# Kernel optimization log

Hardware: AMD Instinct MI355X
Metric: run time of the kernel (lower is better)

## Reference

```python
import jax, jax.numpy as jnp
import numpy as np

N = 100000
E = 3200000
IN_C, H1, H2 = 512, 64, 32


def gcn_norm(edge_index, edge_weight, num_nodes):
    """PyG gcn_norm with add_self_loops=True: D^-1/2 (A+I) D^-1/2 edge weights."""
    row, col = edge_index[0], edge_index[1]
    loop = jnp.arange(num_nodes, dtype=edge_index.dtype)
    row = jnp.concatenate([row, loop])
    col = jnp.concatenate([col, loop])
    w = jnp.concatenate([edge_weight, jnp.ones((num_nodes,), edge_weight.dtype)])
    deg = jax.ops.segment_sum(w, col, num_segments=num_nodes)
    dinv = jnp.where(deg > 0, jax.lax.rsqrt(jnp.maximum(deg, 1e-12)), 0.0)
    wnorm = dinv[row] * w * dinv[col]
    return row, col, wnorm


def gcn_conv(x, W, b, row, col, wnorm, num_nodes):
    h = x @ W                                   # [N, out] linear first (out <= in)
    msg = wnorm[:, None] * h[row]               # gather + per-edge scale  [E+N, out]
    out = jax.ops.segment_sum(msg, col, num_segments=num_nodes)
    return out + b


def setup_inputs() -> dict:
    key = jax.random.key(0)
    ks = jax.random.split(key, 9)
    x = jax.random.normal(ks[0], (N, IN_C), dtype=jnp.float32)
    edge_index = jax.random.randint(ks[1], (2, E), 0, N, dtype=jnp.int64)
    edge_weight = jax.random.uniform(ks[2], (E,), dtype=jnp.float32)
    # Glorot-style init for GCN linear weights, zero bias (PyG defaults).
    def glorot(k, fan_in, fan_out):
        s = np.sqrt(6.0 / (fan_in + fan_out)).astype(np.float32)
        return jax.random.uniform(k, (fan_in, fan_out), jnp.float32, -s, s)
    return {
        "x": x,
        "edge_index": edge_index,
        "edge_weight": edge_weight,
        "W1": glorot(ks[3], IN_C, H1), "b1": jnp.zeros((H1,), jnp.float32),
        "W2": glorot(ks[4], H1, H2),  "b2": jnp.zeros((H2,), jnp.float32),
        "W3": glorot(ks[5], H2, 1),   "b3": jnp.zeros((1,), jnp.float32),
    }


def reference(x, edge_index, edge_weight, W1, b1, W2, b2, W3, b3):
    # Inference mode: dropout is identity (training=False).
    row, col, wnorm = gcn_norm(edge_index, edge_weight, N)  # cached=True: shared across layers
    h = jax.nn.relu(gcn_conv(x, W1, b1, row, col, wnorm, N))
    h = jax.nn.relu(gcn_conv(h, W2, b2, row, col, wnorm, N))
    h = gcn_conv(h, W3, b3, row, col, wnorm, N)
    return h.reshape(-1)  # [N]
```

## Files before the change

kernel.cpp:

```cpp
#include <hip/hip_runtime.h>

constexpr int BLK = 256;
constexpr int NBLKBIN = 512;
constexpr int MAXNB   = 1024;

typedef __bf16 bf16x8 __attribute__((ext_vector_type(8)));
typedef float  f32x4  __attribute__((ext_vector_type(4)));

__device__ __forceinline__ float blo(unsigned u) { return __uint_as_float(u << 16); }
__device__ __forceinline__ float bhi(unsigned u) { return __uint_as_float(u & 0xffff0000u); }

__device__ __forceinline__ int detect64(const void* ei) {
    const int* p = (const int*)ei;
    int is64 = 1;
#pragma unroll
    for (int i = 0; i < 16; ++i)
        if (p[2 * i + 1] != 0) is64 = 0;
    return is64;
}

__device__ __forceinline__ int load_idx(const void* ei, size_t pos, int is64) {
    if (is64) return (int)((const long long*)ei)[pos];
    return ((const int*)ei)[pos];
}

__global__ void k_prep(const float* __restrict__ W1, const float* __restrict__ W2,
                       __bf16* __restrict__ Wtf, __bf16* __restrict__ Wtf2,
                       int* __restrict__ bkt_cnt, int nb) {
    const int b = blockIdx.x;
    const int t = threadIdx.x;
    if (b < 16) {
        int i = b * 256 + t;
        int lane = i & 63;
        int tt   = (i >> 6) & 3;
        int k0c  = i >> 8;
        int col  = tt * 16 + (lane & 15);
        int kbase = k0c * 32 + (lane >> 4) * 8;
        bf16x8 v;
#pragma unroll
        for (int j = 0; j < 8; ++j) v[j] = (__bf16)W1[(size_t)(kbase + j) * 64 + col];
        *(bf16x8*)(Wtf + (size_t)i * 8) = v;
    } else if (b == 16) {
        int i = t;
        int lane = i & 63;
        int ct   = i >> 6;
        int tt = ct & 1, chunk = ct >> 1;
        int col  = tt * 16 + (lane & 15);
        int kbase = chunk * 32 + (lane >> 4) * 8;
        bf16x8 v;
#pragma unroll
        for (int j = 0; j < 8; ++j) v[j] = (__bf16)W2[(size_t)(kbase + j) * 32 + col];
        *(bf16x8*)(Wtf2 + (size_t)i * 8) = v;
    } else {
        for (int i = t; i < nb; i += 256) bkt_cnt[i] = 0;
    }
}

__global__ __launch_bounds__(256) void k_binhist(const void* __restrict__ ei, int e,
                                                 int* __restrict__ bucket_cnt, int nb) {
    __shared__ int hist[MAXNB];
    const int t = threadIdx.x;
    for (int b = t; b < nb; b += 256) hist[b] = 0;
    __syncthreads();
    const int is64 = detect64(ei);
    const int chunk = (e + NBLKBIN - 1) / NBLKBIN;
    const int i0 = blockIdx.x * chunk;
    const int i1 = min(e, i0 + chunk);
    for (int i = i0 + t; i < i1; i += 256) {
        int dst = load_idx(ei, (size_t)e + i, is64);
        atomicAdd(&hist[dst >> 7], 1);
    }
    __syncthreads();
    for (int b = t; b < nb; b += 256) {
        int c = hist[b];
        if (c) atomicAdd(&bucket_cnt[b], c);
    }
}

__global__ void k_scanbkt(const int* __restrict__ cnt, int* __restrict__ offs,
                          int* __restrict__ cursor, int nb, int e) {
    __shared__ int sh[256];
    const int t = threadIdx.x;
    const int base = t * 4;
    int v[4]; int s = 0;
#pragma unroll
    for (int k = 0; k < 4; ++k) {
        int i = base + k;
        v[k] = (i < nb) ? cnt[i] : 0;
        s += v[k];
    }
    sh[t] = s;
    __syncthreads();
    for (int d = 1; d < 256; d <<= 1) {
        int x = (t >= d) ? sh[t - d] : 0;
        __syncthreads();
        sh[t] += x;
        __syncthreads();
    }
    int excl = (t == 0) ? 0 : sh[t - 1];
#pragma unroll
    for (int k = 0; k < 4; ++k) {
        int i = base + k;
        if (i < nb) { offs[i] = excl; cursor[i] = excl; excl += v[k]; }
    }
    if (t == 255) offs[nb] = e;
}

__global__ __launch_bounds__(256) void k_binscatter(const void* __restrict__ ei,
                                                    const float* __restrict__ ew, int e,
                                                    int* __restrict__ bucket_cursor,
                                                    int2* __restrict__ binned, int nb) {
    __shared__ int hist[MAXNB];
    const int t = threadIdx.x;
    for (int b = t; b < nb; b += 256) hist[b] = 0;
    __syncthreads();
    const int is64 = detect64(ei);
    const int chunk = (e + NBLKBIN - 1) / NBLKBIN;
    const int i0 = blockIdx.x * chunk;
    const int i1 = min(e, i0 + chunk);
    for (int i = i0 + t; i < i1; i += 256) {
        int dst = load_idx(ei, (size_t)e + i, is64);
        atomicAdd(&hist[dst >> 7], 1);
    }
    __syncthreads();
    for (int b = t; b < nb; b += 256) {
        int c = hist[b];
        int base = 0;
        if (c) base = atomicAdd(&bucket_cursor[b], c);
        hist[b] = base;
    }
    __syncthreads();
    for (int i = i0 + t; i < i1; i += 256) {
        int dst = load_idx(ei, (size_t)e + i, is64);
        int src = load_idx(ei, (size_t)i, is64);
        float w = ew[i];
        int bin = dst >> 7;
        int pos = atomicAdd(&hist[bin], 1);
        binned[pos] = make_int2(src | ((dst & 127) << 20), __float_as_int(w));
    }
}

__global__ __launch_bounds__(256) void k_bucketcnt(const int* __restrict__ bucket_offs,
                                                   const int2* __restrict__ binned,
                                                   int* __restrict__ counts,
                                                   float* __restrict__ dinv, int n) {
    __shared__ int                icnt[128];
    __shared__ unsigned long long facc[128];
    const int t = threadIdx.x;
    const int k = blockIdx.x;
    if (t < 128) { icnt[t] = 0; facc[t] = 0ull; }
    __syncthreads();
    const int j0 = bucket_offs[k], j1 = bucket_offs[k + 1];
    const float SCALE = 1099511627776.f;
    for (int j = j0 + t; j < j1; j += 256) {
        int2 p = binned[j];
        int dl = ((unsigned)p.x) >> 20;
        atomicAdd(&icnt[dl], 1);
        atomicAdd(&facc[dl], (unsigned long long)(__int_as_float(p.y) * SCALE));
    }
    __syncthreads();
    if (t < 128) {
        int nd = k * 128 + t;
        if (nd < n) {
            counts[nd] = icnt[t];
            float deg = fmaf((float)facc[t], 1.f / 1099511627776.f, 1.0f);
            dinv[nd] = rsqrtf(deg);
        }
    }
}

__global__ void k_scan1(const int* __restrict__ in, int* __restrict__ out,
                        int* __restrict__ bsum, int n) {
    __shared__ int sh[256];
    const int t = threadIdx.x;
    const int base = blockIdx.x * 1024 + t * 4;
    int v[4];
    int s = 0;
#pragma unroll
    for (int k = 0; k < 4; ++k) {
        int i = base + k;
        v[k] = (i < n) ? in[i] : 0;
        s += v[k];
    }
    sh[t] = s;
    __syncthreads();
    for (int d = 1; d < 256; d <<= 1) {
        int x = (t >= d) ? sh[t - d] : 0;
        __syncthreads();
        sh[t] += x;
        __syncthreads();
    }
    int excl = (t == 0) ? 0 : sh[t - 1];
    if (t == 255) bsum[blockIdx.x] = sh[255];
#pragma unroll
    for (int k = 0; k < 4; ++k) {
        int i = base + k;
        if (i < n) { out[i] = excl; excl += v[k]; }
    }
}

__global__ void k_scan2(int* __restrict__ bsum, int nb) {
    __shared__ int sh[128];
    const int t = threadIdx.x;
    sh[t] = (t < nb) ? bsum[t] : 0;
    __syncthreads();
    for (int d = 1; d < 128; d <<= 1) {
        int x = (t >= d) ? sh[t - d] : 0;
        __syncthreads();
        sh[t] += x;
        __syncthreads();
    }
    if (t < nb) bsum[t] = (t == 0) ? 0 : sh[t - 1];
}

__global__ void k_scan3(int* __restrict__ offs, const int* __restrict__ scanned,
                        const int* __restrict__ bsum, int n, int e) {
    long i = (long)blockIdx.x * BLK + threadIdx.x;
    if (i < n) offs[i] = scanned[i] + bsum[i >> 10];
    if (i == 0) offs[n] = e;
}

__global__ __launch_bounds__(256) void k_place(const int* __restrict__ bucket_offs,
                                               const int2* __restrict__ binned,
                                               const int* __restrict__ offs,
                                               const float* __restrict__ dinv,
                                               int2* __restrict__ csrp, int n) {
    __shared__ int cur[128];
    const int t = threadIdx.x;
    const int k = blockIdx.x;
    if (t < 128) {
        int nd = k * 128 + t;
        cur[t] = (nd < n) ? offs[nd] : 0;
    }
    __syncthreads();
    const int j0 = bucket_offs[k], j1 = bucket_offs[k + 1];
    for (int j = j0 + t; j < j1; j += 256) {
        int2 p = binned[j];
        int dl  = ((unsigned)p.x) >> 20;
        int src = p.x & 0xFFFFF;
        int pos = atomicAdd(&cur[dl], 1);
        float w2 = __int_as_float(p.y) * dinv[src];
        csrp[pos] = make_int2(src, __float_as_int(w2));
    }
}

__global__ __launch_bounds__(256) void k_gemm1_mfma(const float* __restrict__ X,
                                                    const __bf16* __restrict__ Wtf,
                                                    __bf16* __restrict__ H, int nrows) {
    const int wave = threadIdx.x >> 6;
    const int lane = threadIdx.x & 63;
    const int l15  = lane & 15;
    const int lq   = lane >> 4;
    const long rbase = (long)blockIdx.x * 128 + wave * 32;

    long ar0 = rbase + l15;      if (ar0 >= nrows) ar0 = nrows - 1;
    long ar1 = rbase + 16 + l15; if (ar1 >= nrows) ar1 = nrows - 1;
    const float4* x0 = (const float4*)(X + (size_t)ar0 * 512) + lq * 2;
    const float4* x1 = (const float4*)(X + (size_t)ar1 * 512) + lq * 2;

    f32x4 acc[2][4];
#pragma unroll
    for (int r = 0; r < 2; ++r)
#pragma unroll
        for (int t = 0; t < 4; ++t) acc[r][t] = f32x4{0.f, 0.f, 0.f, 0.f};

    float4 pa[2][2][2];
#pragma unroll
    for (int s = 0; s < 2; ++s) {
        pa[s][0][0] = x0[s * 8]; pa[s][0][1] = x0[s * 8 + 1];
        pa[s][1][0] = x1[s * 8]; pa[s][1][1] = x1[s * 8 + 1];
    }

#pragma unroll
    for (int k0c = 0; k0c < 16; ++k0c) {
        const int s = k0c & 1;
        float4 a00 = pa[s][0][0], a01 = pa[s][0][1];
        float4 a10 = pa[s][1][0], a11 = pa[s][1][1];
        if (k0c + 2 < 16) {
            pa[s][0][0] = x0[(k0c + 2) * 8]; pa[s][0][1] = x0[(k0c + 2) * 8 + 1];
            pa[s][1][0] = x1[(k0c + 2) * 8]; pa[s][1][1] = x1[(k0c + 2) * 8 + 1];
        }
        bf16x8 af0, af1;
        af0[0] = (__bf16)a00.x; af0[1] = (__bf16)a00.y; af0[2] = (__bf16)a00.z; af0[3] = (__bf16)a00.w;
        af0[4] = (__bf16)a01.x; af0[5] = (__bf16)a01.y; af0[6] = (__bf16)a01.z; af0[7] = (__bf16)a01.w;
        af1[0] = (__bf16)a10.x; af1[1] = (__bf16)a10.y; af1[2] = (__bf16)a10.z; af1[3] = (__bf16)a10.w;
        af1[4] = (__bf16)a11.x; af1[5] = (__bf16)a11.y; af1[6] = (__bf16)a11.z; af1[7] = (__bf16)a11.w;
#pragma unroll
        for (int t = 0; t < 4; ++t) {
            bf16x8 bf_ = *(const bf16x8*)(Wtf + ((size_t)(k0c * 4 + t) * 64 + lane) * 8);
            acc[0][t] = __builtin_amdgcn_mfma_f32_16x16x32_bf16(af0, bf_, acc[0][t], 0, 0, 0);
            acc[1][t] = __builtin_amdgcn_mfma_f32_16x16x32_bf16(af1, bf_, acc[1][t], 0, 0, 0);
        }
    }
#pragma unroll
    for (int rr = 0; rr < 2; ++rr)
#pragma unroll
    for (int t = 0; t < 4; ++t)
#pragma unroll
    for (int r = 0; r < 4; ++r) {
        long row = rbase + rr * 16 + lq * 4 + r;
        if (row < nrows) H[(size_t)row * 64 + t * 16 + l15] = (__bf16)acc[rr][t][r];
    }
}

__global__ __launch_bounds__(256) void k_gemm2_mfma(const __bf16* __restrict__ A,
                                                    const __bf16* __restrict__ Wtf2,
                                                    __bf16* __restrict__ H, int nrows) {
    const int wave = threadIdx.x >> 6;
    const int lane = threadIdx.x & 63;
    const int l15  = lane & 15;
    const int lq   = lane >> 4;
    const long rbase = (long)blockIdx.x * 64 + wave * 16;

    long arow = rbase + l15;
    if (arow >= nrows) arow = nrows - 1;

    f32x4 acc[2] = {{0.f,0.f,0.f,0.f},{0.f,0.f,0.f,0.f}};
#pragma unroll
    for (int c = 0; c < 2; ++c) {
        bf16x8 af = *(const bf16x8*)(A + (size_t)arow * 64 + c * 32 + lq * 8);
#pragma unroll
        for (int t = 0; t < 2; ++t) {
            bf16x8 bf_ = *(const bf16x8*)(Wtf2 + ((size_t)(c * 2 + t) * 64 + lane) * 8);
            acc[t] = __builtin_amdgcn_mfma_f32_16x16x32_bf16(af, bf_, acc[t], 0, 0, 0);
        }
    }
#pragma unroll
    for (int t = 0; t < 2; ++t)
#pragma unroll
    for (int r = 0; r < 4; ++r) {
        long row = rbase + lq * 4 + r;
        if (row < nrows) H[(size_t)row * 32 + t * 16 + l15] = (__bf16)acc[t][r];
    }
}

template <int K, int EPI>
__global__ __launch_bounds__(256) void k_prop_bf(const int* __restrict__ offs,
                                                 const int2* __restrict__ csrp,
                                                 const __bf16* __restrict__ hb,
                                                 const float* __restrict__ dinv,
                                                 const float* __restrict__ bias,
                                                 const float* __restrict__ W3,
                                                 void* __restrict__ outv, int n) {
    constexpr int SUB = K / 4;
    constexpr int NPW = 64 / SUB;
    constexpr int NPB = 4 * NPW;
    const int t    = threadIdx.x;
    const int lane = t & 63;
    const int wave = t >> 6;
    const int chq  = lane & (SUB - 1);
    const int sub  = lane / SUB;
    const long nd  = (long)blockIdx.x * NPB + wave * NPW + sub;
    if (nd >= n) return;

    const unsigned short* h = (const unsigned short*)hb;
    const int j0 = offs[nd], j1 = offs[nd + 1];
    float a0 = 0.f, a1 = 0.f, a2 = 0.f, a3 = 0.f;
    int j = j0;
    for (; j + 3 < j1; j += 4) {
        int2 p0 = csrp[j];
        int2 p1 = csrp[j + 1];
        int2 p2 = csrp[j + 2];
        int2 p3 = csrp[j + 3];
        uint2 u0 = *(const uint2*)(h + (size_t)p0.x * K + 4 * chq);
        uint2 u1 = *(const uint2*)(h + (size_t)p1.x * K + 4 * chq);
        uint2 u2 = *(const uint2*)(h + (size_t)p2.x * K + 4 * chq);
        uint2 u3 = *(const uint2*)(h + (size_t)p3.x * K + 4 * chq);
        float w0 = __int_as_float(p0.y), w1 = __int_as_float(p1.y);
        float w2 = __int_as_float(p2.y), w3 = __int_as_float(p3.y);
        a0 = fmaf(w0, blo(u0.x), a0); a1 = fmaf(w0, bhi(u0.x), a1);
        a2 = fmaf(w0, blo(u0.y), a2); a3 = fmaf(w0, bhi(u0.y), a3);
        a0 = fmaf(w1, blo(u1.x), a0); a1 = fmaf(w1, bhi(u1.x), a1);
        a2 = fmaf(w1, blo(u1.y), a2); a3 = fmaf(w1, bhi(u1.y), a3);
        a0 = fmaf(w2, blo(u2.x), a0); a1 = fmaf(w2, bhi(u2.x), a1);
        a2 = fmaf(w2, blo(u2.y), a2); a3 = fmaf(w2, bhi(u2.y), a3);
        a0 = fmaf(w3, blo(u3.x), a0); a1 = fmaf(w3, bhi(u3.x), a1);
        a2 = fmaf(w3, blo(u3.y), a2); a3 = fmaf(w3, bhi(u3.y), a3);
    }
    for (; j < j1; ++j) {
        int2 p0 = csrp[j];
        uint2 u0 = *(const uint2*)(h + (size_t)p0.x * K + 4 * chq);
        float w0 = __int_as_float(p0.y);
        a0 = fmaf(w0, blo(u0.x), a0); a1 = fmaf(w0, bhi(u0.x), a1);
        a2 = fmaf(w0, blo(u0.y), a2); a3 = fmaf(w0, bhi(u0.y), a3);
    }
    const float di = dinv[nd];
    const float s  = di * di;
    uint2 us = *(const uint2*)(h + (size_t)nd * K + 4 * chq);
    float4 bv = *(const float4*)(bias + 4 * chq);
    float o0 = fmaf(di, a0, fmaf(s, blo(us.x), bv.x));
    float o1 = fmaf(di, a1, fmaf(s, bhi(us.x), bv.y));
    float o2 = fmaf(di, a2, fmaf(s, blo(us.y), bv.z));
    float o3 = fmaf(di, a3, fmaf(s, bhi(us.y), bv.w));
    o0 = fmaxf(o0, 0.f); o1 = fmaxf(o1, 0.f); o2 = fmaxf(o2, 0.f); o3 = fmaxf(o3, 0.f);
    if (EPI == 0) {
        unsigned short s0 = __builtin_bit_cast(unsigned short, (__bf16)o0);
        unsigned short s1 = __builtin_bit_cast(unsigned short, (__bf16)o1);
        unsigned short s2 = __builtin_bit_cast(unsigned short, (__bf16)o2);
        unsigned short s3 = __builtin_bit_cast(unsigned short, (__bf16)o3);
        uint2 pk;
        pk.x = (unsigned)s0 | ((unsigned)s1 << 16);
        pk.y = (unsigned)s2 | ((unsigned)s3 << 16);
        *(uint2*)((unsigned*)outv + (size_t)nd * (K / 2) + 2 * chq) = pk;
    } else {
        float4 wv = *(const float4*)(W3 + 4 * chq);
        float part = o0 * wv.x + o1 * wv.y + o2 * wv.z + o3 * wv.w;
#pragma unroll
        for (int d = SUB / 2; d >= 1; d >>= 1) part += __shfl_xor(part, d, SUB);
        if (chq == 0) ((float*)outv)[nd] = part;
    }
}

__global__ __launch_bounds__(256) void k_prop1(const int* __restrict__ offs,
                                               const int2* __restrict__ csrp,
                                               const float* __restrict__ h,
                                               const float* __restrict__ dinv,
                                               const float* __restrict__ bias,
                                               float* __restrict__ out, int n) {
    long nd = (long)blockIdx.x * BLK + threadIdx.x;
    if (nd >= n) return;
    const int j0 = offs[nd], j1 = offs[nd + 1];
    float acc = 0.f;
    int j = j0;
    for (; j + 3 < j1; j += 4) {
        int2 p0 = csrp[j];
        int2 p1 = csrp[j + 1];
        int2 p2 = csrp[j + 2];
        int2 p3 = csrp[j + 3];
        acc = fmaf(__int_as_float(p0.y), h[p0.x], acc);
        acc = fmaf(__int_as_float(p1.y), h[p1.x], acc);
        acc = fmaf(__int_as_float(p2.y), h[p2.x], acc);
        acc = fmaf(__int_as_float(p3.y), h[p3.x], acc);
    }
    for (; j < j1; ++j) {
        int2 p0 = csrp[j];
        acc = fmaf(__int_as_float(p0.y), h[p0.x], acc);
    }
    const float di = dinv[nd];
    out[nd] = fmaf(di, acc, fmaf(di * di, h[nd], bias[0]));
}

extern "C" void kernel_launch(void* const* d_in, const int* in_sizes, int n_in,
                              void* d_out, int out_size, void* d_ws, size_t ws_size,
                              hipStream_t stream) {
    const float* x  = (const float*)d_in[0];
    const void*  ei = d_in[1];
    const float* ew = (const float*)d_in[2];
    const float* W1 = (const float*)d_in[3];
    const float* b1 = (const float*)d_in[4];
    const float* W2 = (const float*)d_in[5];
    const float* b2 = (const float*)d_in[6];
    const float* W3 = (const float*)d_in[7];
    const float* b3 = (const float*)d_in[8];
    float* out = (float*)d_out;

    const int n = in_sizes[0] / 512;
    const int e = in_sizes[2];
    const int nb = (n + 127) >> 7;

    char* ws = (char*)d_ws;
    size_t off = 0;
    auto alloc = [&](size_t bytes) {
        void* p = ws + off;
        off = (off + bytes + 255) & ~(size_t)255;
        return p;
    };
    int2*   binned   = (int2*)  alloc((size_t)e * 8);
    __bf16* hbuf1    = (__bf16*)binned;
    int*    bkt_cnt  = (int*)   alloc((size_t)(MAXNB + 1) * 4);
    int*    bkt_offs = (int*)   alloc((size_t)(MAXNB + 1) * 4);
    int*    bkt_cur  = (int*)   alloc((size_t)(MAXNB + 1) * 4);
    int*    counts   = (int*)   alloc((size_t)n * 4);
    int*    offs     = (int*)   alloc((size_t)(n + 1) * 4);
    int*    bsum     = (int*)   alloc(512);
    int2*   csrp     = (int2*)  alloc((size_t)e * 8);
    float*  dinv     = (float*) alloc((size_t)n * 4);
    __bf16* pb64     = (__bf16*)alloc((size_t)n * 64 * 2);
    __bf16* hbuf2    = (__bf16*)alloc((size_t)n * 32 * 2);
    float*  h3       = (float*) alloc((size_t)n * 4);
    __bf16* Wtf      = (__bf16*)alloc((size_t)512 * 64 * 2);
    __bf16* Wtf2     = (__bf16*)alloc((size_t)64 * 32 * 2);
    (void)ws_size; (void)n_in; (void)out_size;

    const int gb_n = (n + BLK - 1) / BLK;
    const int nb_scan = (n + 1023) / 1024;

    k_prep<<<18, 256, 0, stream>>>(W1, W2, Wtf, Wtf2, bkt_cnt, nb);
    k_binhist<<<NBLKBIN, 256, 0, stream>>>(ei, e, bkt_cnt, nb);
    k_scanbkt<<<1, 256, 0, stream>>>(bkt_cnt, bkt_offs, bkt_cur, nb, e);
    k_binscatter<<<NBLKBIN, 256, 0, stream>>>(ei, ew, e, bkt_cur, binned, nb);
    k_bucketcnt<<<nb, 256, 0, stream>>>(bkt_offs, binned, counts, dinv, n);
    k_scan1<<<nb_scan, 256, 0, stream>>>(counts, counts, bsum, n);
    k_scan2<<<1, 128, 0, stream>>>(bsum, nb_scan);
    k_scan3<<<gb_n, BLK, 0, stream>>>(offs, counts, bsum, n, e);
    k_place<<<nb, 256, 0, stream>>>(bkt_offs, binned, offs, dinv, csrp, n);

    k_gemm1_mfma<<<(n + 127) / 128, 256, 0, stream>>>(x, Wtf, hbuf1, n);
    k_prop_bf<64, 0><<<(n + 15) / 16, 256, 0, stream>>>(offs, csrp, hbuf1, dinv, b1, nullptr, pb64, n);

    k_gemm2_mfma<<<(n + 63) / 64, 256, 0, stream>>>(pb64, Wtf2, hbuf2, n);
    k_prop_bf<32, 1><<<(n + 31) / 32, 256, 0, stream>>>(offs, csrp, hbuf2, dinv, b2, W3, h3, n);

    k_prop1<<<gb_n, BLK, 0, stream>>>(offs, csrp, h3, dinv, b3, out, n);
}
```

Measured before the change: 349.0 us.

## Fuse CSR build into one kernel and fold source dinv into GEMM outputs

Merges the bucket count, three-kernel global scan and placement into a single per-bucket kernel. Because buckets are contiguous in the binned array, each bucket's offsets come from its own start plus a local 128-entry scan. The source-side D^-1/2 scaling moves out of the per-edge weights and into the GEMM epilogues (and the layer-3 projection), so CSR placement no longer needs a random gather of dinv per edge. This removes four launches and a global counts pass. The trade-off is that the pre-scaled features are rounded to bf16, which slightly changes numerics.

```diff
diff --git a/kernel.cpp b/kernel.cpp
--- a/kernel.cpp
+++ b/kernel.cpp
@@ -140,17 +140,20 @@
     }
 }
 
-__global__ __launch_bounds__(256) void k_bucketcnt(const int* __restrict__ bucket_offs,
-                                                   const int2* __restrict__ binned,
-                                                   int* __restrict__ counts,
-                                                   float* __restrict__ dinv, int n) {
+__global__ __launch_bounds__(256) void k_build(const int* __restrict__ bkt_offs,
+                                               const int2* __restrict__ binned,
+                                               float* __restrict__ dinv,
+                                               int* __restrict__ offs,
+                                               int2* __restrict__ csrp, int n, int e) {
     __shared__ int                icnt[128];
     __shared__ unsigned long long facc[128];
+    __shared__ int                scn[128];
+    __shared__ int                cur[128];
     const int t = threadIdx.x;
-    const int k = blockIdx.x;
+    const int b = blockIdx.x;
     if (t < 128) { icnt[t] = 0; facc[t] = 0ull; }
     __syncthreads();
-    const int j0 = bucket_offs[k], j1 = bucket_offs[k + 1];
+    const int j0 = bkt_offs[b], j1 = bkt_offs[b + 1];
     const float SCALE = 1099511627776.f;
     for (int j = j0 + t; j < j1; j += 256) {
         int2 p = binned[j];
@@ -160,92 +163,39 @@
     }
     __syncthreads();
     if (t < 128) {
-        int nd = k * 128 + t;
-        if (nd < n) {
-            counts[nd] = icnt[t];
-            float deg = fmaf((float)facc[t], 1.f / 1099511627776.f, 1.0f);
-            dinv[nd] = rsqrtf(deg);
-        }
-    }
-}
-
-__global__ void k_scan1(const int* __restrict__ in, int* __restrict__ out,
-                        int* __restrict__ bsum, int n) {
-    __shared__ int sh[256];
-    const int t = threadIdx.x;
-    const int base = blockIdx.x * 1024 + t * 4;
-    int v[4];
-    int s = 0;
-#pragma unroll
-    for (int k = 0; k < 4; ++k) {
-        int i = base + k;
-        v[k] = (i < n) ? in[i] : 0;
-        s += v[k];
-    }
-    sh[t] = s;
-    __syncthreads();
-    for (int d = 1; d < 256; d <<= 1) {
-        int x = (t >= d) ? sh[t - d] : 0;
+        int nd = b * 128 + t;
+        if (nd < n) dinv[nd] = rsqrtf(fmaf((float)facc[t], 1.f / 1099511627776.f, 1.0f));
+        scn[t] = icnt[t];
+    }
+    __syncthreads();
+    for (int d = 1; d < 128; d <<= 1) {
+        int x = 0;
+        if (t < 128 && t >= d) x = scn[t - d];
         __syncthreads();
-        sh[t] += x;
+        if (t < 128) scn[t] += x;
         __syncthreads();
     }
-    int excl = (t == 0) ? 0 : sh[t - 1];
-    if (t == 255) bsum[blockIdx.x] = sh[255];
-#pragma unroll
-    for (int k = 0; k < 4; ++k) {
-        int i = base + k;
-        if (i < n) { out[i] = excl; excl += v[k]; }
-    }
-}
-
-__global__ void k_scan2(int* __restrict__ bsum, int nb) {
-    __shared__ int sh[128];
-    const int t = threadIdx.x;
-    sh[t] = (t < nb) ? bsum[t] : 0;
-    __syncthreads();
-    for (int d = 1; d < 128; d <<= 1) {
-        int x = (t >= d) ? sh[t - d] : 0;
-        __syncthreads();
-        sh[t] += x;
-        __syncthreads();
-    }
-    if (t < nb) bsum[t] = (t == 0) ? 0 : sh[t - 1];
-}
-
-__global__ void k_scan3(int* __restrict__ offs, const int* __restrict__ scanned,
-                        const int* __restrict__ bsum, int n, int e) {
-    long i = (long)blockIdx.x * BLK + threadIdx.x;
-    if (i < n) offs[i] = scanned[i] + bsum[i >> 10];
-    if (i == 0) offs[n] = e;
-}
-
-__global__ __launch_bounds__(256) void k_place(const int* __restrict__ bucket_offs,
-                                               const int2* __restrict__ binned,
-                                               const int* __restrict__ offs,
-                                               const float* __restrict__ dinv,
-                                               int2* __restrict__ csrp, int n) {
-    __shared__ int cur[128];
-    const int t = threadIdx.x;
-    const int k = blockIdx.x;
     if (t < 128) {
-        int nd = k * 128 + t;
-        cur[t] = (nd < n) ? offs[nd] : 0;
-    }
-    __syncthreads();
-    const int j0 = bucket_offs[k], j1 = bucket_offs[k + 1];
+        int excl = (t == 0) ? 0 : scn[t - 1];
+        int abs0 = j0 + excl;
+        cur[t] = abs0;
+        int nd = b * 128 + t;
+        if (nd < n) offs[nd] = abs0;
+    }
+    if (b == 0 && t == 0) offs[n] = e;
+    __syncthreads();
     for (int j = j0 + t; j < j1; j += 256) {
         int2 p = binned[j];
         int dl  = ((unsigned)p.x) >> 20;
         int src = p.x & 0xFFFFF;
         int pos = atomicAdd(&cur[dl], 1);
-        float w2 = __int_as_float(p.y) * dinv[src];
-        csrp[pos] = make_int2(src, __float_as_int(w2));
+        csrp[pos] = make_int2(src, p.y);
     }
 }
 
 __global__ __launch_bounds__(256) void k_gemm1_mfma(const float* __restrict__ X,
                                                     const __bf16* __restrict__ Wtf,
+                                                    const float* __restrict__ dinv,
                                                     __bf16* __restrict__ H, int nrows) {
     const int wave = threadIdx.x >> 6;
     const int lane = threadIdx.x & 63;
@@ -295,16 +245,20 @@
 #pragma unroll
     for (int rr = 0; rr < 2; ++rr)
 #pragma unroll
-    for (int t = 0; t < 4; ++t)
-#pragma unroll
     for (int r = 0; r < 4; ++r) {
         long row = rbase + rr * 16 + lq * 4 + r;
-        if (row < nrows) H[(size_t)row * 64 + t * 16 + l15] = (__bf16)acc[rr][t][r];
+        if (row < nrows) {
+            float dv = dinv[row];
+#pragma unroll
+            for (int t = 0; t < 4; ++t)
+                H[(size_t)row * 64 + t * 16 + l15] = (__bf16)(acc[rr][t][r] * dv);
+        }
     }
 }
 
 __global__ __launch_bounds__(256) void k_gemm2_mfma(const __bf16* __restrict__ A,
                                                     const __bf16* __restrict__ Wtf2,
+                                                    const float* __restrict__ dinv,
                                                     __bf16* __restrict__ H, int nrows) {
     const int wave = threadIdx.x >> 6;
     const int lane = threadIdx.x & 63;
@@ -326,11 +280,14 @@
         }
     }
 #pragma unroll
-    for (int t = 0; t < 2; ++t)
-#pragma unroll
     for (int r = 0; r < 4; ++r) {
         long row = rbase + lq * 4 + r;
-        if (row < nrows) H[(size_t)row * 32 + t * 16 + l15] = (__bf16)acc[t][r];
+        if (row < nrows) {
+            float dv = dinv[row];
+#pragma unroll
+            for (int t = 0; t < 2; ++t)
+                H[(size_t)row * 32 + t * 16 + l15] = (__bf16)(acc[t][r] * dv);
+        }
     }
 }
 
@@ -385,13 +342,12 @@
         a2 = fmaf(w0, blo(u0.y), a2); a3 = fmaf(w0, bhi(u0.y), a3);
     }
     const float di = dinv[nd];
-    const float s  = di * di;
     uint2 us = *(const uint2*)(h + (size_t)nd * K + 4 * chq);
     float4 bv = *(const float4*)(bias + 4 * chq);
-    float o0 = fmaf(di, a0, fmaf(s, blo(us.x), bv.x));
-    float o1 = fmaf(di, a1, fmaf(s, bhi(us.x), bv.y));
-    float o2 = fmaf(di, a2, fmaf(s, blo(us.y), bv.z));
-    float o3 = fmaf(di, a3, fmaf(s, bhi(us.y), bv.w));
+    float o0 = fmaf(di, a0 + blo(us.x), bv.x);
+    float o1 = fmaf(di, a1 + bhi(us.x), bv.y);
+    float o2 = fmaf(di, a2 + blo(us.y), bv.z);
+    float o3 = fmaf(di, a3 + bhi(us.y), bv.w);
     o0 = fmaxf(o0, 0.f); o1 = fmaxf(o1, 0.f); o2 = fmaxf(o2, 0.f); o3 = fmaxf(o3, 0.f);
     if (EPI == 0) {
         unsigned short s0 = __builtin_bit_cast(unsigned short, (__bf16)o0);
@@ -407,7 +363,7 @@
         float part = o0 * wv.x + o1 * wv.y + o2 * wv.z + o3 * wv.w;
 #pragma unroll
         for (int d = SUB / 2; d >= 1; d >>= 1) part += __shfl_xor(part, d, SUB);
-        if (chq == 0) ((float*)outv)[nd] = part;
+        if (chq == 0) ((float*)outv)[nd] = di * part;
     }
 }
 
@@ -437,7 +393,7 @@
         acc = fmaf(__int_as_float(p0.y), h[p0.x], acc);
     }
     const float di = dinv[nd];
-    out[nd] = fmaf(di, acc, fmaf(di * di, h[nd], bias[0]));
+    out[nd] = fmaf(di, acc + h[nd], bias[0]);
 }
 
 extern "C" void kernel_launch(void* const* d_in, const int* in_sizes, int n_in,
@@ -470,9 +426,7 @@
     int*    bkt_cnt  = (int*)   alloc((size_t)(MAXNB + 1) * 4);
     int*    bkt_offs = (int*)   alloc((size_t)(MAXNB + 1) * 4);
     int*    bkt_cur  = (int*)   alloc((size_t)(MAXNB + 1) * 4);
-    int*    counts   = (int*)   alloc((size_t)n * 4);
     int*    offs     = (int*)   alloc((size_t)(n + 1) * 4);
-    int*    bsum     = (int*)   alloc(512);
     int2*   csrp     = (int2*)  alloc((size_t)e * 8);
     float*  dinv     = (float*) alloc((size_t)n * 4);
     __bf16* pb64     = (__bf16*)alloc((size_t)n * 64 * 2);
@@ -483,22 +437,17 @@
     (void)ws_size; (void)n_in; (void)out_size;
 
     const int gb_n = (n + BLK - 1) / BLK;
-    const int nb_scan = (n + 1023) / 1024;
 
     k_prep<<<18, 256, 0, stream>>>(W1, W2, Wtf, Wtf2, bkt_cnt, nb);
     k_binhist<<<NBLKBIN, 256, 0, stream>>>(ei, e, bkt_cnt, nb);
     k_scanbkt<<<1, 256, 0, stream>>>(bkt_cnt, bkt_offs, bkt_cur, nb, e);
     k_binscatter<<<NBLKBIN, 256, 0, stream>>>(ei, ew, e, bkt_cur, binned, nb);
-    k_bucketcnt<<<nb, 256, 0, stream>>>(bkt_offs, binned, counts, dinv, n);
-    k_scan1<<<nb_scan, 256, 0, stream>>>(counts, counts, bsum, n);
-    k_scan2<<<1, 128, 0, stream>>>(bsum, nb_scan);
-    k_scan3<<<gb_n, BLK, 0, stream>>>(offs, counts, bsum, n, e);
-    k_place<<<nb, 256, 0, stream>>>(bkt_offs, binned, offs, dinv, csrp, n);
-
-    k_gemm1_mfma<<<(n + 127) / 128, 256, 0, stream>>>(x, Wtf, hbuf1, n);
+    k_build<<<nb, 256, 0, stream>>>(bkt_offs, binned, dinv, offs, csrp, n, e);
+
+    k_gemm1_mfma<<<(n + 127) / 128, 256, 0, stream>>>(x, Wtf, dinv, hbuf1, n);
     k_prop_bf<64, 0><<<(n + 15) / 16, 256, 0, stream>>>(offs, csrp, hbuf1, dinv, b1, nullptr, pb64, n);
 
-    k_gemm2_mfma<<<(n + 63) / 64, 256, 0, stream>>>(pb64, Wtf2, hbuf2, n);
+    k_gemm2_mfma<<<(n + 63) / 64, 256, 0, stream>>>(pb64, Wtf2, dinv, hbuf2, n);
     k_prop_bf<32, 1><<<(n + 31) / 32, 256, 0, stream>>>(offs, csrp, hbuf2, dinv, b2, W3, h3, n);
 
     k_prop1<<<gb_n, BLK, 0, stream>>>(offs, csrp, h3, dinv, b3, out, n);
```

Measured after the change: 326.9 us. 6.3% less time.
